# Performance work log

Hardware: AMD Instinct MI355X
Metric: run time of the kernel (lower is better)

The kernel has to match this reference:

```python
import jax, jax.numpy as jnp
import numpy as np

N_NODES = 20000
N_EDGES = 320000
EMB = 256
K_DIFF = 3
BN_EPS = 1e-5


def conv1d(x, w, b, stride):
    # x: [N, Cin, L], w: [Cout, Cin, K]
    y = jax.lax.conv_general_dilated(x, w, window_strides=(stride,), padding='VALID',
                                     dimension_numbers=('NCH', 'OIH', 'NCH'))
    return y + b[None, :, None]


def batchnorm_train(x, gamma, beta):
    # training-mode BatchNorm1d over (N, L) per channel, biased variance
    m = jnp.mean(x, axis=(0, 2), keepdims=True)
    v = jnp.var(x, axis=(0, 2), keepdims=True)
    return (x - m) * jax.lax.rsqrt(v + BN_EPS) * gamma[None, :, None] + beta[None, :, None]


def dconv(X, W, b, row, col, norm_out, norm_in, n):
    # Diffusion convolution (pytorch_geometric_temporal DConv), K hops,
    # forward (out-degree) and backward (in-degree) random walks.
    def prop(x, norm):
        msg = norm[:, None] * x[row]                    # [E, F] gather
        return jax.ops.segment_sum(msg, col, num_segments=n)  # scatter-add to targets

    K = W.shape[1]
    Tx_0 = X
    Tx_1 = X
    H = X @ W[0, 0] + X @ W[1, 0]
    if K > 1:
        Tx_1_o = prop(X, norm_out)
        Tx_1_i = prop(X, norm_in)
        H = H + Tx_1_o @ W[0, 1] + Tx_1_i @ W[1, 1]
    for k in range(2, K):
        Tx_2_o = 2.0 * prop(Tx_1_o, norm_out) - Tx_0
        Tx_2_i = 2.0 * prop(Tx_1_i, norm_in) - Tx_0
        H = H + Tx_2_o @ W[0, k] + Tx_2_i @ W[1, k]
        Tx_0, Tx_1_o, Tx_1_i = Tx_1, Tx_2_o, Tx_2_i
    return H + b


def setup_inputs() -> dict:
    key = jax.random.key(0)
    ks = jax.random.split(key, 16)
    d_in = 2 * EMB  # concat([X, H])
    inp = {
        'x': jax.random.normal(ks[0], (N_NODES, 1, 100), dtype=jnp.float32),
        'edge_index': jax.random.randint(ks[1], (2, N_EDGES), 0, N_NODES, dtype=jnp.int32),
        'hidden_state': jax.random.normal(ks[2], (N_NODES, EMB), dtype=jnp.float32),
        'conv1_w': jax.random.normal(ks[3], (32, 1, 10), dtype=jnp.float32) * 0.2,
        'conv1_b': jnp.zeros((32,), jnp.float32),
        'bn1_gamma': jnp.ones((32,), jnp.float32),
        'bn1_beta': jnp.zeros((32,), jnp.float32),
        'conv2_w': jax.random.normal(ks[4], (32, 32, 10), dtype=jnp.float32) * 0.05,
        'conv2_b': jnp.zeros((32,), jnp.float32),
        'bn2_gamma': jnp.ones((32,), jnp.float32),
        'bn2_beta': jnp.zeros((32,), jnp.float32),
        'W_z': jax.random.normal(ks[5], (2, K_DIFF, d_in, EMB), dtype=jnp.float32) * 0.05,
        'b_z': jnp.zeros((EMB,), jnp.float32),
        'W_r': jax.random.normal(ks[6], (2, K_DIFF, d_in, EMB), dtype=jnp.float32) * 0.05,
        'b_r': jnp.zeros((EMB,), jnp.float32),
        'W_h': jax.random.normal(ks[7], (2, K_DIFF, d_in, EMB), dtype=jnp.float32) * 0.05,
        'b_h': jnp.zeros((EMB,), jnp.float32),
    }
    return inp


def reference(x, edge_index, hidden_state, conv1_w, conv1_b, bn1_gamma, bn1_beta,
              conv2_w, conv2_b, bn2_gamma, bn2_beta, W_z, b_z, W_r, b_r, W_h, b_h):
    n = x.shape[0]
    # CNN embedding: conv -> relu -> bn, twice
    h = batchnorm_train(jax.nn.relu(conv1d(x, conv1_w, conv1_b, 3)), bn1_gamma, bn1_beta)
    h = batchnorm_train(jax.nn.relu(conv1d(h, conv2_w, conv2_b, 3)), bn2_gamma, bn2_beta)
    X = h.reshape(n, -1)  # [N, EMB]

    row, col = edge_index[0], edge_index[1]
    ones = jnp.ones((row.shape[0],), X.dtype)
    deg_out = jax.ops.segment_sum(ones, row, num_segments=n)
    deg_in = jax.ops.segment_sum(ones, col, num_segments=n)
    norm_out = (1.0 / deg_out)[row]
    norm_in = (1.0 / deg_in)[col]

    H0 = hidden_state
    XH = jnp.concatenate([X, H0], axis=1)
    Z = jax.nn.sigmoid(dconv(XH, W_z, b_z, row, col, norm_out, norm_in, n))
    R = jax.nn.sigmoid(dconv(XH, W_r, b_r, row, col, norm_out, norm_in, n))
    XRH = jnp.concatenate([X, R * H0], axis=1)
    H_tilde = jnp.tanh(dconv(XRH, W_h, b_h, row, col, norm_out, norm_in, n))
    H = Z * H0 + (1.0 - Z) * H_tilde
    return jax.nn.relu(H)
```

## Files before the change

kernel.cpp:

```cpp
#include <hip/hip_runtime.h>
#include <cstdint>
#include <cstddef>

#define NN 20000
#define NE 320000
#define SBUF 10240000

typedef float f32x4 __attribute__((ext_vector_type(4)));
typedef short s16x8 __attribute__((ext_vector_type(8)));
typedef unsigned short us;

__device__ __forceinline__ us f2bf(float x){
    unsigned u = __float_as_uint(x);
    unsigned r = (u + 0x7fffu + ((u >> 16) & 1u)) >> 16;
    return (us)r;
}
__device__ __forceinline__ float bf2f(us s){
    return __uint_as_float(((unsigned)s) << 16);
}

__device__ __forceinline__ void gl16(const void* g, void* l){
    __builtin_amdgcn_global_load_lds((const __attribute__((address_space(1))) unsigned int*)g,
                                     (__attribute__((address_space(3))) unsigned int*)l, 16, 0, 0);
}

__device__ __forceinline__ void upd8(uint4 v, float w, float* ao, float* ai){
    float f0=__uint_as_float(v.x<<16), f1=__uint_as_float(v.x&0xffff0000u);
    float f2=__uint_as_float(v.y<<16), f3=__uint_as_float(v.y&0xffff0000u);
    float f4=__uint_as_float(v.z<<16), f5=__uint_as_float(v.z&0xffff0000u);
    float f6=__uint_as_float(v.w<<16), f7=__uint_as_float(v.w&0xffff0000u);
    ao[0]=fmaf(w,f0,ao[0]); ao[1]=fmaf(w,f1,ao[1]); ao[2]=fmaf(w,f2,ao[2]); ao[3]=fmaf(w,f3,ao[3]);
    ao[4]=fmaf(w,f4,ao[4]); ao[5]=fmaf(w,f5,ao[5]); ao[6]=fmaf(w,f6,ao[6]); ao[7]=fmaf(w,f7,ao[7]);
    ai[0]+=f0; ai[1]+=f1; ai[2]+=f2; ai[3]+=f3; ai[4]+=f4; ai[5]+=f5; ai[6]+=f6; ai[7]+=f7;
}
__device__ __forceinline__ void updw(uint4 v, float w, float* a){
    float f0=__uint_as_float(v.x<<16), f1=__uint_as_float(v.x&0xffff0000u);
    float f2=__uint_as_float(v.y<<16), f3=__uint_as_float(v.y&0xffff0000u);
    float f4=__uint_as_float(v.z<<16), f5=__uint_as_float(v.z&0xffff0000u);
    float f6=__uint_as_float(v.w<<16), f7=__uint_as_float(v.w&0xffff0000u);
    a[0]=fmaf(w,f0,a[0]); a[1]=fmaf(w,f1,a[1]); a[2]=fmaf(w,f2,a[2]); a[3]=fmaf(w,f3,a[3]);
    a[4]=fmaf(w,f4,a[4]); a[5]=fmaf(w,f5,a[5]); a[6]=fmaf(w,f6,a[6]); a[7]=fmaf(w,f7,a[7]);
}
__device__ __forceinline__ uint4 pack8(const float* a){
    uint4 r;
    r.x=((unsigned)f2bf(a[1])<<16)|f2bf(a[0]);
    r.y=((unsigned)f2bf(a[3])<<16)|f2bf(a[2]);
    r.z=((unsigned)f2bf(a[5])<<16)|f2bf(a[4]);
    r.w=((unsigned)f2bf(a[7])<<16)|f2bf(a[6]);
    return r;
}
__device__ __forceinline__ uint4 pack8s(const float* a, float s){
    uint4 r;
    r.x=((unsigned)f2bf(s*a[1])<<16)|f2bf(s*a[0]);
    r.y=((unsigned)f2bf(s*a[3])<<16)|f2bf(s*a[2]);
    r.z=((unsigned)f2bf(s*a[5])<<16)|f2bf(s*a[4]);
    r.w=((unsigned)f2bf(s*a[7])<<16)|f2bf(s*a[6]);
    return r;
}


__global__ void k_zero(uint32_t* p, int n){
    int i = blockIdx.x*256 + threadIdx.x;
    if(i < n) p[i] = 0u;
}

__global__ void k_degree(const int* __restrict__ ei, int* degout, int* degin){
    int e = blockIdx.x*256 + threadIdx.x;
    if(e < NE){
        atomicAdd(&degout[ei[e]], 1);
        atomicAdd(&degin[ei[NE+e]], 1);
    }
}

__global__ void k_scan(const int* __restrict__ degin, int* __restrict__ coloff,
                       float* __restrict__ invdegin){
    __shared__ int part[1024];
    int t = threadIdx.x;
    int base = t*20;
    int s = 0;
    for(int k=0;k<20;k++){ int i = base+k; if(i < NN) s += degin[i]; }
    part[t] = s;
    __syncthreads();
    for(int off=1; off<1024; off<<=1){
        int v = (t>=off) ? part[t-off] : 0;
        __syncthreads();
        part[t] += v;
        __syncthreads();
    }
    int run = (t>0) ? part[t-1] : 0;
    for(int k=0;k<20;k++){
        int i = base+k;
        if(i < NN){
            int d = degin[i];
            coloff[i] = run;
            run += d;
            invdegin[i] = (d>0) ? (1.0f/(float)d) : 0.0f;
        }
    }
    if(t==1023) coloff[NN] = part[1023];
}

__global__ void k_csr(const int* __restrict__ ei, const int* __restrict__ degout,
                      const int* __restrict__ coloff, int* cnt, int2* __restrict__ ew){
    int e = blockIdx.x*256 + threadIdx.x;
    if(e < NE){
        int r = ei[e], c = ei[NE+e];
        int pos = coloff[c] + atomicAdd(&cnt[c], 1);
        int2 v; v.x = r; v.y = __float_as_int(1.0f/(float)degout[r]);
        ew[pos] = v;
    }
}


__global__ void k_conv1(const float* __restrict__ x, const float* __restrict__ w1,
                        const float* __restrict__ b1, us* __restrict__ y1T){
    __shared__ float w[320];
    __shared__ float bb[32];
    int t = threadIdx.x;
    for(int i=t;i<320;i+=256) w[i] = w1[i];
    if(t < 32) bb[t] = b1[t];
    __syncthreads();
    int gid = blockIdx.x*256 + t;
    int node = gid>>5, p = gid&31;
    us* yo = y1T + (size_t)node*1024 + p*32;
    if(p >= 31){
        uint4 z = {0,0,0,0};
        *(uint4*)yo = z; *(uint4*)(yo+8) = z;
        *(uint4*)(yo+16) = z; *(uint4*)(yo+24) = z;
        return;
    }
    const float* xr = x + node*100 + 3*p;
    float xv[10];
    #pragma unroll
    for(int k=0;k<10;k++) xv[k] = xr[k];
    float o[32];
    #pragma unroll
    for(int c=0;c<32;c++){
        float a = bb[c];
        #pragma unroll
        for(int k=0;k<10;k++) a = fmaf(w[c*10+k], xv[k], a);
        o[c] = fmaxf(a, 0.0f);
    }
    *(uint4*)yo      = pack8(o);
    *(uint4*)(yo+8)  = pack8(o+8);
    *(uint4*)(yo+16) = pack8(o+16);
    *(uint4*)(yo+24) = pack8(o+24);
}

__global__ void k_chanstats_T(const us* __restrict__ y, float* __restrict__ sq){
    int tid = blockIdx.x*256 + threadIdx.x;
    int slot = tid & 1023;
    int c = slot & 31;
    int node0 = tid >> 10;
    float s = 0.f, q = 0.f;
    for(int n=node0; n<NN; n+=64){
        float v = bf2f(y[(size_t)n*1024 + slot]);
        s += v; q = fmaf(v, v, q);
    }
    s += __shfl_xor(s, 32);
    q += __shfl_xor(q, 32);
    if((threadIdx.x & 63) < 32){
        atomicAdd(&sq[c], s);
        atomicAdd(&sq[32+c], q);
    }
}

template<int SLOTS, int PPC>
__global__ void k_chanstats_bf(const us* __restrict__ y, float* __restrict__ sq){
    int tid = blockIdx.x*blockDim.x + threadIdx.x;
    int slot = tid & (SLOTS-1);
    int node0 = tid / SLOTS;
    int nstride = (gridDim.x*blockDim.x) / SLOTS;
    int c = slot / PPC;
    float s = 0.f, q = 0.f;
    for(int n=node0; n<NN; n+=nstride){
        float v = bf2f(y[(size_t)n*SLOTS + slot]);
        s += v; q = fmaf(v, v, q);
    }
    #pragma unroll
    for(int m=PPC>>1; m>0; m>>=1){
        s += __shfl_xor(s, m);
        q += __shfl_xor(q, m);
    }
    if((threadIdx.x & (PPC-1)) == 0){
        atomicAdd(&sq[c], s);
        atomicAdd(&sq[32+c], q);
    }
}

__global__ void k_bnfin(const float* __restrict__ sq, const float* __restrict__ gamma,
                        const float* __restrict__ beta, float* __restrict__ scsh,
                        float inv_count){
    int c = threadIdx.x;
    if(c < 32){
        float m = sq[c]*inv_count;
        float v = sq[32+c]*inv_count - m*m;
        float sc = gamma[c]*rsqrtf(v + 1e-5f);
        scsh[c] = sc;
        scsh[32+c] = beta[c] - m*sc;
    }
}

__global__ void k_wprep(const float* __restrict__ w2, const float* __restrict__ scsh1,
                        const float* __restrict__ b2, us* __restrict__ Bf,
                        float* __restrict__ biasc){
    int b = blockIdx.x;
    int t = threadIdx.x;
    if(b < 40){
        int idx = b*256 + t;
        int kk = idx >> 10, c2 = (idx >> 5) & 31, c = idx & 31;
        Bf[idx] = f2bf(scsh1[c] * w2[c2*320 + c*10 + kk]);
    }else{
        int c2 = t >> 3, part = t & 7;
        float s = 0.f;
        for(int i=part; i<320; i+=8)
            s += scsh1[32 + i/10] * w2[c2*320 + i];
        s += __shfl_xor(s,1); s += __shfl_xor(s,2); s += __shfl_xor(s,4);
        if(part == 0) biasc[c2] = b2[c2] + s;
    }
}

__global__ void __launch_bounds__(256) k_conv2m(const us* __restrict__ y1T,
        const us* __restrict__ Bf, const float* __restrict__ biasc,
        us* __restrict__ Xpre){
    int t = threadIdx.x;
    int wv = t>>6, l = t&63;
    int l15 = l&15, g = l>>4;
    int r0 = blockIdx.x*64 + wv*16;
    int arow = r0 + l15;
    int an = arow>>3, ap = arow&7;
    const us* abase = y1T + (size_t)an*1024 + (3*ap)*32 + g*8;
    const us* bbase = Bf + (size_t)l15*32 + g*8;
    f32x4 acc0 = {}, acc1 = {};
    #pragma unroll
    for(int kk=0;kk<10;kk++){
        s16x8 af = *(const s16x8*)(abase + kk*32);
        s16x8 b0 = *(const s16x8*)(bbase + kk*1024);
        s16x8 b1 = *(const s16x8*)(bbase + kk*1024 + 512);
        acc0 = __builtin_amdgcn_mfma_f32_16x16x32_bf16(af, b0, acc0, 0, 0, 0);
        acc1 = __builtin_amdgcn_mfma_f32_16x16x32_bf16(af, b1, acc1, 0, 0, 0);
    }
    int base = r0 + g*4;
    int n = base>>3, p0 = base&7;
    #pragma unroll
    for(int nf=0;nf<2;nf++){
        int c2 = nf*16 + l15;
        float bb = biasc[c2];
        f32x4 a = nf ? acc1 : acc0;
        float v0 = fmaxf(a[0]+bb,0.f), v1 = fmaxf(a[1]+bb,0.f);
        float v2 = fmaxf(a[2]+bb,0.f), v3 = fmaxf(a[3]+bb,0.f);
        uint2 pk;
        pk.x = ((unsigned)f2bf(v1)<<16)|f2bf(v0);
        pk.y = ((unsigned)f2bf(v3)<<16)|f2bf(v2);
        *(uint2*)&Xpre[(size_t)n*256 + c2*8 + p0] = pk;
    }
}

__global__ void __launch_bounds__(256) k_prep(const us* __restrict__ Xpre,
        const float* __restrict__ scsh, const float* __restrict__ h0,
        us* __restrict__ XHp){
    int node = blockIdx.x*4 + (threadIdx.x>>6);
    if(node >= NN) return;
    int lane = threadIdx.x & 63;
    int half = lane>>5, g = lane&31;
    uint4 o;
    if(half == 0){
        uint4 v = *(const uint4*)(Xpre + (size_t)node*256 + g*8);
        float sc = scsh[g], sh = scsh[32+g];
        float y[8];
        y[0]=fmaf(sc,__uint_as_float(v.x<<16),sh); y[1]=fmaf(sc,__uint_as_float(v.x&0xffff0000u),sh);
        y[2]=fmaf(sc,__uint_as_float(v.y<<16),sh); y[3]=fmaf(sc,__uint_as_float(v.y&0xffff0000u),sh);
        y[4]=fmaf(sc,__uint_as_float(v.z<<16),sh); y[5]=fmaf(sc,__uint_as_float(v.z&0xffff0000u),sh);
        y[6]=fmaf(sc,__uint_as_float(v.w<<16),sh); y[7]=fmaf(sc,__uint_as_float(v.w&0xffff0000u),sh);
        o = pack8(y);
    }else{
        float4 a = *(const float4*)(h0 + (size_t)node*256 + g*8);
        float4 b = *(const float4*)(h0 + (size_t)node*256 + g*8 + 4);
        float y[8] = {a.x,a.y,a.z,a.w,b.x,b.y,b.z,b.w};
        o = pack8(y);
    }
    *(uint4*)(XHp + (size_t)node*512 + (size_t)g*16 + half*8) = o;
}


__device__ __forceinline__ float weff_val(const float* W, int term, size_t base){
    const size_t S = 512*256;
    if(term==0)      return W[0*S+base] + W[3*S+base] - W[2*S+base] - W[5*S+base];
    else if(term==1) return W[1*S+base];
    else if(term==2) return W[4*S+base];
    else if(term==3) return 2.0f*W[2*S+base];
    else             return 2.0f*W[5*S+base];
}

template<int NCOL>
__global__ void __launch_bounds__(256) k_wefft(const float* __restrict__ Wa,
        const float* __restrict__ Wb, us* __restrict__ Wt){
    __shared__ float tile[64*65];
    int bx = blockIdx.x;
    constexpr int CT = NCOL/64;
    int kb = bx / (CT*4);
    int rem = bx % (CT*4);
    int ct = rem >> 2, rt = rem & 3;
    int col0 = ct*64, rr0 = rt*64;
    const float* W = (col0 < 256) ? Wa : Wb;
    int jb = col0 & 255;
    int term = kb >> 1, half = kb & 1;
    int t = threadIdx.x;
    int j_l = t & 63, r4 = t >> 6;
    #pragma unroll
    for(int it=0; it<16; it++){
        int rr_l = it*4 + r4;
        int row = half*256 + rr0 + rr_l;
        size_t base = (size_t)row*256 + jb + j_l;
        tile[j_l*65 + rr_l] = weff_val(W, term, base);
    }
    __syncthreads();
    int rr_w = t & 63;
    #pragma unroll
    for(int it=0; it<16; it++){
        int col_l = it*4 + r4;
        Wt[(size_t)(col0+col_l)*2560 + kb*256 + rr0 + rr_w] = f2bf(tile[col_l*65 + rr_w]);
    }
}


__global__ void __launch_bounds__(256) k_prop1(const us* __restrict__ XHp,
        const int* __restrict__ coloff, const int2* __restrict__ ew,
        const float* __restrict__ invdeg, us* __restrict__ T1op, us* __restrict__ T1ip){
    int node = blockIdx.x*4 + (threadIdx.x>>6);
    if(node >= NN) return;
    int lane = threadIdx.x & 63;
    size_t lo = (size_t)(lane&31)*16 + (lane>>5)*8;
    int s = __builtin_amdgcn_readfirstlane(coloff[node]);
    int e = __builtin_amdgcn_readfirstlane(coloff[node+1]);
    float ao[8]={0,0,0,0,0,0,0,0}, ai[8]={0,0,0,0,0,0,0,0};
    int j = s;
    for(; j+7 < e; j += 8){
        int2 ed[8]; uint4 v[8];
        #pragma unroll
        for(int i=0;i<8;i++) ed[i] = ew[j+i];
        #pragma unroll
        for(int i=0;i<8;i++) v[i] = *(const uint4*)(XHp+(size_t)ed[i].x*512+lo);
        #pragma unroll
        for(int i=0;i<8;i++) upd8(v[i], __int_as_float(ed[i].y), ao, ai);
    }
    for(; j < e; j++){
        int2 ed = ew[j];
        uint4 v = *(const uint4*)(XHp+(size_t)ed.x*512+lo);
        upd8(v, __int_as_float(ed.y), ao, ai);
    }
    float wi = invdeg[node];
    *(uint4*)(T1op+(size_t)node*512+lo) = pack8(ao);
    *(uint4*)(T1ip+(size_t)node*512+lo) = pack8s(ai,wi);
}

__global__ void __launch_bounds__(256) k_prop2(const us* __restrict__ T1op,
        const us* __restrict__ T1ip,
        const int* __restrict__ coloff, const int2* __restrict__ ew,
        const float* __restrict__ invdeg, us* __restrict__ P2op, us* __restrict__ P2ip){
    int node = blockIdx.x*4 + (threadIdx.x>>6);
    if(node >= NN) return;
    int lane = threadIdx.x & 63;
    size_t lo = (size_t)(lane&31)*16 + (lane>>5)*8;
    int s = __builtin_amdgcn_readfirstlane(coloff[node]);
    int e = __builtin_amdgcn_readfirstlane(coloff[node+1]);
    float ao[8]={0,0,0,0,0,0,0,0}, ai[8]={0,0,0,0,0,0,0,0};
    int j = s;
    for(; j+3 < e; j += 4){
        int2 ed[4]; uint4 va[4], vb[4];
        #pragma unroll
        for(int i=0;i<4;i++) ed[i] = ew[j+i];
        #pragma unroll
        for(int i=0;i<4;i++){
            size_t o = (size_t)ed[i].x*512+lo;
            va[i] = *(const uint4*)(T1op+o);
            vb[i] = *(const uint4*)(T1ip+o);
        }
        #pragma unroll
        for(int i=0;i<4;i++){
            updw(va[i], __int_as_float(ed[i].y), ao);
            updw(vb[i], 1.0f, ai);
        }
    }
    for(; j < e; j++){
        int2 ed = ew[j];
        size_t o = (size_t)ed.x*512+lo;
        updw(*(const uint4*)(T1op+o), __int_as_float(ed.y), ao);
        updw(*(const uint4*)(T1ip+o), 1.0f, ai);
    }
    float wi = invdeg[node];
    *(uint4*)(P2op+(size_t)node*512+lo) = pack8(ao);
    *(uint4*)(P2ip+(size_t)node*512+lo) = pack8s(ai,wi);
}

__global__ void __launch_bounds__(256) k_propq1(const us* __restrict__ RHb,
        const int* __restrict__ coloff, const int2* __restrict__ ew,
        const float* __restrict__ invdeg, us* __restrict__ Q1p){
    int node = blockIdx.x*4 + (threadIdx.x>>6);
    if(node >= NN) return;
    int lane = threadIdx.x & 63;
    int half = lane>>5, g = lane&31;
    int s = __builtin_amdgcn_readfirstlane(coloff[node]);
    int e = __builtin_amdgcn_readfirstlane(coloff[node+1]);
    float ao[8]={0,0,0,0,0,0,0,0}, ai[8]={0,0,0,0,0,0,0,0};
    int j = s;
    for(; j+3 < e; j += 4){
        int2 e0 = ew[j+half], e1 = ew[j+2+half];
        uint4 v0 = *(const uint4*)(RHb+(size_t)e0.x*256+g*8);
        uint4 v1 = *(const uint4*)(RHb+(size_t)e1.x*256+g*8);
        upd8(v0, __int_as_float(e0.y), ao, ai);
        upd8(v1, __int_as_float(e1.y), ao, ai);
    }
    for(; j+1 < e; j += 2){
        int2 ed = ew[j+half];
        uint4 v = *(const uint4*)(RHb+(size_t)ed.x*256+g*8);
        upd8(v, __int_as_float(ed.y), ao, ai);
    }
    if(j < e && half == 0){
        int2 ed = ew[j];
        uint4 v = *(const uint4*)(RHb+(size_t)ed.x*256+g*8);
        upd8(v, __int_as_float(ed.y), ao, ai);
    }
    #pragma unroll
    for(int k=0;k<8;k++){
        ao[k] += __shfl_xor(ao[k],32);
        ai[k] += __shfl_xor(ai[k],32);
    }
    if(half == 0){
        float wi = invdeg[node];
        *(uint4*)(Q1p+(size_t)node*512+(size_t)g*16)   = pack8(ao);
        *(uint4*)(Q1p+(size_t)node*512+(size_t)g*16+8) = pack8s(ai,wi);
    }
}

__global__ void __launch_bounds__(256) k_propu(const us* __restrict__ Yin,
        const int* __restrict__ coloff, const int2* __restrict__ ew,
        const float* __restrict__ invdeg, us* __restrict__ Pout){
    int node = blockIdx.x*4 + (threadIdx.x>>6);
    if(node >= NN) return;
    int lane = threadIdx.x & 63;
    int half = lane>>5;
    size_t lo = (size_t)(lane&31)*16 + half*8;
    int s = __builtin_amdgcn_readfirstlane(coloff[node]);
    int e = __builtin_amdgcn_readfirstlane(coloff[node+1]);
    float a[8]={0,0,0,0,0,0,0,0};
    int j = s;
    for(; j+7 < e; j += 8){
        int2 ed[8]; uint4 v[8];
        #pragma unroll
        for(int i=0;i<8;i++) ed[i] = ew[j+i];
        #pragma unroll
        for(int i=0;i<8;i++) v[i] = *(const uint4*)(Yin+(size_t)ed[i].x*512+lo);
        #pragma unroll
        for(int i=0;i<8;i++) updw(v[i], half ? 1.0f : __int_as_float(ed[i].y), a);
    }
    for(; j < e; j++){
        int2 ed = ew[j];
        uint4 v = *(const uint4*)(Yin+(size_t)ed.x*512+lo);
        updw(v, half ? 1.0f : __int_as_float(ed.y), a);
    }
    float sc = half ? invdeg[node] : 1.0f;
    *(uint4*)(Pout+(size_t)node*512+lo) = pack8s(a,sc);
}


template<int MODE, int BNT>
__global__ void __launch_bounds__(256) k_gemm(const us* __restrict__ XG,
        const us* __restrict__ RG, const us* __restrict__ Wt,
        const float* __restrict__ bias0, const float* __restrict__ bias1,
        const float* __restrict__ h0, const float* __restrict__ Zin,
        float* __restrict__ out0, us* __restrict__ out1){
    constexpr int WN = BNT/32;
    constexpr int NB = BNT/64;
    __shared__ us As[2][4096];
    __shared__ us Bs[2][BNT*32];
    int t = threadIdx.x;
    int wid = t >> 6, lane = t & 63;
    int l15 = lane & 15, kg = lane >> 4;

    int bid = blockIdx.x;
    int xcd = bid & 7, sblk = bid >> 3;
    int cidx = sblk & 3, r = (sblk >> 2)*8 + xcd;
    if(r >= 157) return;
    int row0 = r*128, col0 = cidx*BNT;
    int rowbase = (wid >> 1)*64, colbase = (wid & 1)*(BNT/2);
    int swz = (l15 >> 1) & 3;

    int srA[2], sgA[2];
    size_t rowoffA[2];
    #pragma unroll
    for(int i=0;i<2;i++){
        int c = t + i*256;
        srA[i] = c >> 2;
        sgA[i] = (c & 3) ^ ((srA[i] >> 1) & 3);
        int gr = row0 + srA[i];
        gr = (gr < NN) ? gr : NN-1;
        rowoffA[i] = (size_t)gr*512 + (size_t)sgA[i]*16;
    }
    int srB[NB], sgB[NB];
    size_t coloffB[NB];
    #pragma unroll
    for(int i=0;i<NB;i++){
        int c = t + i*256;
        srB[i] = c >> 2;
        sgB[i] = (c & 3) ^ ((srB[i] >> 1) & 3);
        coloffB[i] = (size_t)(col0+srB[i])*2560 + (size_t)sgB[i]*8;
    }

    f32x4 acc[4][WN] = {};

    auto stage = [&](int buf, int s){
        int kb = s >> 3;
        int ktc = (s & 7) * 4;
        if(MODE == 1 && kb == 1){
            #pragma unroll
            for(int i=0;i<2;i++)
                gl16(RG + (rowoffA[i] >> 1) + (size_t)ktc*8, &As[buf][(t+i*256)*8]);
        }else{
            const us* Ap;
            if(MODE == 0){
                Ap = XG + (size_t)(kb >> 1) * SBUF + (size_t)(kb & 1) * 8;
            }else{
                if((kb & 1) == 0) Ap = XG + (size_t)(kb >> 1) * SBUF;
                else Ap = RG + (size_t)((kb + 1) >> 2) * SBUF + (size_t)(((kb + 1) >> 1) & 1) * 8;
            }
            #pragma unroll
            for(int i=0;i<2;i++)
                gl16(Ap + rowoffA[i] + (size_t)ktc*16, &As[buf][(t+i*256)*8]);
        }
        const us* Wp = Wt + (size_t)kb*256 + (s & 7)*32;
        #pragma unroll
        for(int i=0;i<NB;i++)
            gl16(Wp + coloffB[i], &Bs[buf][(t+i*256)*8]);
    };

    stage(0, 0);
    stage(1, 1);
    for(int step=0; step<80; ++step){
        int cur = step & 1;
        if(step < 79){
            if(MODE == 0) asm volatile("s_waitcnt vmcnt(4)" ::: "memory");
            else          asm volatile("s_waitcnt vmcnt(3)" ::: "memory");
        }else{
            asm volatile("s_waitcnt vmcnt(0)" ::: "memory");
        }
        __builtin_amdgcn_s_barrier();
        s16x8 af[4], bfr[WN];
        #pragma unroll
        for(int i=0;i<4;i++){
            int row = rowbase + i*16 + l15;
            af[i] = *(const s16x8*)&As[cur][(row*4 + (kg ^ swz))*8];
        }
        #pragma unroll
        for(int n=0;n<WN;n++){
            int colr = colbase + n*16 + l15;
            bfr[n] = *(const s16x8*)&Bs[cur][(colr*4 + (kg ^ swz))*8];
        }
        asm volatile("s_waitcnt lgkmcnt(0)" ::: "memory");
        __builtin_amdgcn_sched_barrier(0);
        __builtin_amdgcn_s_barrier();
        if(step < 78) stage(cur, step+2);
        __builtin_amdgcn_s_setprio(1);
        #pragma unroll
        for(int mi=0;mi<4;mi++){
            #pragma unroll
            for(int ni=0;ni<WN;ni++){
                acc[mi][ni] = __builtin_amdgcn_mfma_f32_16x16x32_bf16(
                    af[mi], bfr[ni], acc[mi][ni], 0, 0, 0);
            }
        }
        __builtin_amdgcn_s_setprio(0);
    }

    #pragma unroll
    for(int mi=0;mi<4;mi++){
        int gr0 = row0 + rowbase + mi*16 + kg*4;
        #pragma unroll
        for(int ni=0;ni<WN;ni++){
            int j = col0 + colbase + ni*16 + l15;
            #pragma unroll
            for(int rr=0;rr<4;rr++){
                int gr = gr0 + rr;
                if(gr < NN){
                    float a = acc[mi][ni][rr];
                    if(MODE == 0){
                        if(j < 256){
                            out0[(size_t)gr*256 + j] = 1.0f/(1.0f + expf(-(a + bias0[j])));
                        }else{
                            int jj = j - 256;
                            float rv = 1.0f/(1.0f + expf(-(a + bias1[jj])));
                            out1[(size_t)gr*256 + jj] = f2bf(rv * h0[(size_t)gr*256 + jj]);
                        }
                    }else{
                        float z = Zin[(size_t)gr*256 + j];
                        float ht = tanhf(a + bias0[j]);
                        float H = z*h0[(size_t)gr*256 + j] + (1.0f - z)*ht;
                        out0[(size_t)gr*256 + j] = fmaxf(H, 0.0f);
                    }
                }
            }
        }
    }
}


extern "C" void kernel_launch(void* const* d_in, const int* in_sizes, int n_in,
                              void* d_out, int out_size, void* d_ws, size_t ws_size,
                              hipStream_t stream){
    const float* x   = (const float*)d_in[0];
    const int*   ei  = (const int*)  d_in[1];
    const float* h0  = (const float*)d_in[2];
    const float* w1  = (const float*)d_in[3];
    const float* b1  = (const float*)d_in[4];
    const float* g1  = (const float*)d_in[5];
    const float* be1 = (const float*)d_in[6];
    const float* w2  = (const float*)d_in[7];
    const float* b2  = (const float*)d_in[8];
    const float* g2  = (const float*)d_in[9];
    const float* be2 = (const float*)d_in[10];
    const float* Wz  = (const float*)d_in[11];
    const float* bz  = (const float*)d_in[12];
    const float* Wr  = (const float*)d_in[13];
    const float* br  = (const float*)d_in[14];
    const float* Wh  = (const float*)d_in[15];
    const float* bh  = (const float*)d_in[16];
    float* out = (float*)d_out;
    float* wsf = (float*)d_ws;
    (void)in_sizes; (void)n_in; (void)out_size;

    const size_t O_DEGO=0, O_DEGI=20000, O_CNT=40000, O_BN=60000;
    const size_t O_COLOFF=60288, O_EW=80384, O_INVDEG=720384;
    const size_t O_WTZR=740480, O_WTH=1395840;
    const size_t O_XPRE=1723520;
    const size_t O_XG=4283520;
    const size_t O_RG=29883520;
    const size_t O_Z=45243520;
    const size_t O_BF=50363520;
    const size_t WS_NEED_BYTES = (size_t)50366080 * 4;
    if(ws_size < WS_NEED_BYTES) return;

    const size_t SW = 5120000;

    int* degout = (int*)(wsf + O_DEGO);
    int* degin  = (int*)(wsf + O_DEGI);
    int* cnt    = (int*)(wsf + O_CNT);
    float* bn   = wsf + O_BN;
    int* coloff = (int*)(wsf + O_COLOFF);
    int2* ew    = (int2*)(wsf + O_EW);
    float* invdeg = wsf + O_INVDEG;
    us* Wtzr = (us*)(wsf + O_WTZR);
    us* Wth  = (us*)(wsf + O_WTH);
    us* Xpre = (us*)(wsf + O_XPRE);
    us* XG   = (us*)(wsf + O_XG);
    us* RG   = (us*)(wsf + O_RG);
    us* XHp  = XG;
    us* T1op = (us*)(wsf + O_XG + SW);
    us* T1ip = (us*)(wsf + O_XG + 2*SW);
    us* P2op = (us*)(wsf + O_XG + 3*SW);
    us* P2ip = (us*)(wsf + O_XG + 4*SW);
    us* RHb  = RG;
    us* Q1p  = (us*)(wsf + O_RG + SW);
    us* Q2p  = (us*)(wsf + O_RG + 2*SW);
    float* Z = wsf + O_Z;
    us* Bf   = (us*)(wsf + O_BF);
    us* y1T  = T1op;

    k_zero<<<236,256,0,stream>>>((uint32_t*)(wsf + O_DEGO), 60256);
    k_degree<<<1250,256,0,stream>>>(ei, degout, degin);
    k_scan<<<1,1024,0,stream>>>(degin, coloff, invdeg);
    k_csr<<<1250,256,0,stream>>>(ei, degout, coloff, cnt, ew);

    k_conv1<<<2500,256,0,stream>>>(x, w1, b1, y1T);
    k_chanstats_T<<<256,256,0,stream>>>(y1T, bn+0);
    k_bnfin<<<1,32,0,stream>>>(bn+0, g1, be1, bn+64, 1.0f/620000.0f);
    k_wprep<<<41,256,0,stream>>>(w2, bn+64, b2, Bf, bn+256);
    k_conv2m<<<2500,256,0,stream>>>(y1T, Bf, bn+256, Xpre);
    k_chanstats_bf<256,8><<<64,256,0,stream>>>(Xpre, bn+128);
    k_bnfin<<<1,32,0,stream>>>(bn+128, g2, be2, bn+192, 1.0f/160000.0f);
    k_prep<<<5000,256,0,stream>>>(Xpre, bn+192, h0, XHp);

    k_wefft<512><<<320,256,0,stream>>>(Wz, Wr, Wtzr);
    k_wefft<256><<<160,256,0,stream>>>(Wh, Wh, Wth);

    k_prop1<<<5000,256,0,stream>>>(XHp, coloff, ew, invdeg, T1op, T1ip);
    k_prop2<<<5000,256,0,stream>>>(T1op, T1ip, coloff, ew, invdeg, P2op, P2ip);

    k_gemm<0,128><<<640,256,0,stream>>>(XG, RG, Wtzr, bz, br, h0, nullptr, Z, RHb);

    k_propq1<<<5000,256,0,stream>>>(RHb, coloff, ew, invdeg, Q1p);
    k_propu<<<5000,256,0,stream>>>(Q1p, coloff, ew, invdeg, Q2p);

    k_gemm<1,64><<<640,256,0,stream>>>(XG, RG, Wth, bh, nullptr, h0, Z, out, nullptr);
}
```

Before: 707.0 us.

## Widen GEMM tiles to 512-thread blocks covering twice the output columns

The two fused gate GEMM kernels now launch 512-thread blocks, each computing a 128-row by 256- or 128-column tile instead of 256-thread blocks over half as many columns. The grid is halved and the warp-to-subtile mapping is rearranged. Each A tile is therefore loaded once per two former column blocks, which cuts global and LDS staging traffic for the activations, and the vmcnt waits are adjusted for the reduced per-thread load count. In exchange, each CU holds fewer, larger blocks, which may lower occupancy and load balance with only 320 blocks.

```diff
diff --git a/kernel.cpp b/kernel.cpp
--- a/kernel.cpp
+++ b/kernel.cpp
@@ -464,44 +464,37 @@
 }
 
 
-template<int MODE, int BNT>
-__global__ void __launch_bounds__(256) k_gemm(const us* __restrict__ XG,
+template<int MODE, int COLS>
+__global__ void __launch_bounds__(512) k_gemm(const us* __restrict__ XG,
         const us* __restrict__ RG, const us* __restrict__ Wt,
         const float* __restrict__ bias0, const float* __restrict__ bias1,
         const float* __restrict__ h0, const float* __restrict__ Zin,
         float* __restrict__ out0, us* __restrict__ out1){
-    constexpr int WN = BNT/32;
-    constexpr int NB = BNT/64;
+    constexpr int WN = COLS/64;
+    constexpr int NBB = COLS/128;
     __shared__ us As[2][4096];
-    __shared__ us Bs[2][BNT*32];
+    __shared__ us Bs[2][COLS*32];
     int t = threadIdx.x;
     int wid = t >> 6, lane = t & 63;
     int l15 = lane & 15, kg = lane >> 4;
 
     int bid = blockIdx.x;
     int xcd = bid & 7, sblk = bid >> 3;
-    int cidx = sblk & 3, r = (sblk >> 2)*8 + xcd;
+    int cidx = sblk & 1, r = (sblk >> 1)*8 + xcd;
     if(r >= 157) return;
-    int row0 = r*128, col0 = cidx*BNT;
-    int rowbase = (wid >> 1)*64, colbase = (wid & 1)*(BNT/2);
+    int row0 = r*128, col0 = cidx*COLS;
+    int rowbase = (wid & 1)*64, colbase = (wid >> 1)*(WN*16);
     int swz = (l15 >> 1) & 3;
 
-    int srA[2], sgA[2];
-    size_t rowoffA[2];
-    #pragma unroll
-    for(int i=0;i<2;i++){
-        int c = t + i*256;
-        srA[i] = c >> 2;
-        sgA[i] = (c & 3) ^ ((srA[i] >> 1) & 3);
-        int gr = row0 + srA[i];
-        gr = (gr < NN) ? gr : NN-1;
-        rowoffA[i] = (size_t)gr*512 + (size_t)sgA[i]*16;
-    }
-    int srB[NB], sgB[NB];
-    size_t coloffB[NB];
-    #pragma unroll
-    for(int i=0;i<NB;i++){
-        int c = t + i*256;
+    int srA = t >> 2;
+    int sgA = (t & 3) ^ ((srA >> 1) & 3);
+    int grA = row0 + srA; grA = (grA < NN) ? grA : NN-1;
+    size_t rowoffA = (size_t)grA*512 + (size_t)sgA*16;
+    int srB[NBB], sgB[NBB];
+    size_t coloffB[NBB];
+    #pragma unroll
+    for(int i=0;i<NBB;i++){
+        int c = t + i*512;
         srB[i] = c >> 2;
         sgB[i] = (c & 3) ^ ((srB[i] >> 1) & 3);
         coloffB[i] = (size_t)(col0+srB[i])*2560 + (size_t)sgB[i]*8;
@@ -513,9 +506,7 @@
         int kb = s >> 3;
         int ktc = (s & 7) * 4;
         if(MODE == 1 && kb == 1){
-            #pragma unroll
-            for(int i=0;i<2;i++)
-                gl16(RG + (rowoffA[i] >> 1) + (size_t)ktc*8, &As[buf][(t+i*256)*8]);
+            gl16(RG + (rowoffA >> 1) + (size_t)ktc*8, &As[buf][t*8]);
         }else{
             const us* Ap;
             if(MODE == 0){
@@ -524,14 +515,12 @@
                 if((kb & 1) == 0) Ap = XG + (size_t)(kb >> 1) * SBUF;
                 else Ap = RG + (size_t)((kb + 1) >> 2) * SBUF + (size_t)(((kb + 1) >> 1) & 1) * 8;
             }
-            #pragma unroll
-            for(int i=0;i<2;i++)
-                gl16(Ap + rowoffA[i] + (size_t)ktc*16, &As[buf][(t+i*256)*8]);
+            gl16(Ap + rowoffA + (size_t)ktc*16, &As[buf][t*8]);
         }
         const us* Wp = Wt + (size_t)kb*256 + (s & 7)*32;
         #pragma unroll
-        for(int i=0;i<NB;i++)
-            gl16(Wp + coloffB[i], &Bs[buf][(t+i*256)*8]);
+        for(int i=0;i<NBB;i++)
+            gl16(Wp + coloffB[i], &Bs[buf][(t+i*512)*8]);
     };
 
     stage(0, 0);
@@ -539,8 +528,8 @@
     for(int step=0; step<80; ++step){
         int cur = step & 1;
         if(step < 79){
-            if(MODE == 0) asm volatile("s_waitcnt vmcnt(4)" ::: "memory");
-            else          asm volatile("s_waitcnt vmcnt(3)" ::: "memory");
+            if(MODE == 0) asm volatile("s_waitcnt vmcnt(3)" ::: "memory");
+            else          asm volatile("s_waitcnt vmcnt(2)" ::: "memory");
         }else{
             asm volatile("s_waitcnt vmcnt(0)" ::: "memory");
         }
@@ -685,10 +674,10 @@
     k_prop1<<<5000,256,0,stream>>>(XHp, coloff, ew, invdeg, T1op, T1ip);
     k_prop2<<<5000,256,0,stream>>>(T1op, T1ip, coloff, ew, invdeg, P2op, P2ip);
 
-    k_gemm<0,128><<<640,256,0,stream>>>(XG, RG, Wtzr, bz, br, h0, nullptr, Z, RHb);
+    k_gemm<0,256><<<320,512,0,stream>>>(XG, RG, Wtzr, bz, br, h0, nullptr, Z, RHb);
 
     k_propq1<<<5000,256,0,stream>>>(RHb, coloff, ew, invdeg, Q1p);
     k_propu<<<5000,256,0,stream>>>(Q1p, coloff, ew, invdeg, Q2p);
 
-    k_gemm<1,64><<<640,256,0,stream>>>(XG, RG, Wth, bh, nullptr, h0, Z, out, nullptr);
-}
+    k_gemm<1,128><<<320,512,0,stream>>>(XG, RG, Wth, bh, nullptr, h0, Z, out, nullptr);
+}
```

Result: no change. 710.3 us (+0.5%).
